# Optimization experiments

Hardware: AMD Instinct MI355X
Metric: run time of the kernel (lower is better)

Reference implementation:

```python
import jax, jax.numpy as jnp
import numpy as np

T, N, F, H, C, E, K = 8, 100000, 64, 64, 16, 1250000, 2


def setup_inputs() -> dict:
    key = jax.random.key(0)
    ks = jax.random.split(key, 18)
    s = 0.05
    inp = {
        'X_seq': jax.random.normal(ks[0], (T, N, F), jnp.float32),
        'edge_index': jax.random.randint(ks[1], (2, E), 0, N, dtype=jnp.int64),
    }
    # 6 ChebConvs: (x_z, h_z, x_r, h_r, x_h, h_h); weight (K, in, out), bias (out,)
    names_in = [('Wxz', F), ('Whz', H), ('Wxr', F), ('Whr', H), ('Wxh', F), ('Whh', H)]
    for i, (nm, cin) in enumerate(names_in):
        inp[nm] = jax.random.normal(ks[2 + 2 * i], (K, cin, H), jnp.float32) * s
        inp['b' + nm[1:]] = jnp.zeros((H,), jnp.float32)
    inp['Wlin'] = jax.random.normal(ks[14], (H, C), jnp.float32) * s
    inp['blin'] = jnp.zeros((C,), jnp.float32)
    return inp


def _cheb(x, W, b, mv):
    # ChebConv, sym normalization, lambda_max=2: L_tilde = -D^{-1/2} A D^{-1/2}
    out = x @ W[0]
    if W.shape[0] > 1:
        Tx_prev, Tx = x, mv(x)
        out = out + Tx @ W[1]
        for k in range(2, W.shape[0]):
            Tx_prev, Tx = Tx, 2.0 * mv(Tx) - Tx_prev
            out = out + Tx @ W[k]
    return out + b


def reference(X_seq, edge_index, Wxz, bxz, Whz, bhz, Wxr, bxr, Whr, bhr,
              Wxh, bxh, Whh, bhh, Wlin, blin):
    src, dst = edge_index[0], edge_index[1]
    n = X_seq.shape[1]
    deg = jax.ops.segment_sum(jnp.ones_like(src, jnp.float32), src, num_segments=n)
    dinv = jnp.where(deg > 0, jax.lax.rsqrt(jnp.maximum(deg, 1.0)), 0.0)
    w = -dinv[src] * dinv[dst]  # scaled Laplacian off-diagonal (diag is 0)

    def mv(x):  # L_tilde @ x via edge gather/scatter
        return jax.ops.segment_sum(w[:, None] * x[src], dst, num_segments=n)

    def step(h, x_t):
        z = jax.nn.sigmoid(_cheb(x_t, Wxz, bxz, mv) + _cheb(h, Whz, bhz, mv))
        r = jax.nn.sigmoid(_cheb(x_t, Wxr, bxr, mv) + _cheb(h, Whr, bhr, mv))
        h_tilde = jnp.tanh(_cheb(x_t, Wxh, bxh, mv) + _cheb(h * r, Whh, bhh, mv))
        h = z * h + (1.0 - z) * h_tilde
        return h, None

    h0 = jnp.zeros((n, Whz.shape[2]), X_seq.dtype)
    h, _ = jax.lax.scan(step, h0, X_seq)
    return h @ Wlin + blin
```

## Files before the change

kernel.cpp:

```cpp
#include <hip/hip_runtime.h>
#include <math.h>

#define T_STEPS 8
#define F_DIM 64

using half8 = __attribute__((ext_vector_type(8))) _Float16;
using half4 = __attribute__((ext_vector_type(4))) _Float16;
using f32x4 = __attribute__((ext_vector_type(4))) float;

__device__ __forceinline__ float sigmoidf_(float x) { return 1.f / (1.f + __expf(-x)); }


__global__ void k_deg_cnt(const int* ei, int E, int N, int* deg, int* cnt) {
  int e = blockIdx.x * blockDim.x + threadIdx.x;
  if (e >= E) return;
  int s = ei[e];
  int d = ei[E + e];
  if ((unsigned)s < (unsigned)N) atomicAdd(&deg[s], 1);
  if ((unsigned)d < (unsigned)N) atomicAdd(&cnt[d], 1);
}

__global__ void k_dinv(const int* deg, float* dinv, int n) {
  int i = blockIdx.x * blockDim.x + threadIdx.x;
  if (i >= n) return;
  int d = deg[i];
  dinv[i] = d > 0 ? 1.0f / sqrtf((float)d) : 0.f;
}

__global__ void k_scan1(const int* cnt, int* incl, int* bsum, int n) {
  __shared__ int s[1024];
  int t = threadIdx.x;
  int i = blockIdx.x * 1024 + t;
  int v = (i < n) ? cnt[i] : 0;
  s[t] = v;
  __syncthreads();
  for (int off = 1; off < 1024; off <<= 1) {
    int add = (t >= off) ? s[t - off] : 0;
    __syncthreads();
    s[t] += add;
    __syncthreads();
  }
  if (i < n) incl[i] = s[t];
  if (t == 1023) bsum[blockIdx.x] = s[1023];
}

__global__ void k_scan2(const int* bsum, int* boff, int nb) {
  if (threadIdx.x == 0 && blockIdx.x == 0) {
    int run = 0;
    for (int b = 0; b < nb; ++b) { int v = bsum[b]; boff[b] = run; run += v; }
  }
}

__global__ void k_scan3(const int* incl, const int* cnt, const int* boff,
                        int* rp, int n, int E) {
  int i = blockIdx.x * 1024 + threadIdx.x;
  if (i >= n) return;
  int b = i >> 10;
  rp[i] = incl[i] - cnt[i] + boff[b];
  if (i == n - 1) rp[n] = incl[i] + boff[b];
}

__global__ void k_fill(const int* ei, int E, int N, const float* dinv,
                       const int* rp, int* fill, int* col, float* wv) {
  int e = blockIdx.x * blockDim.x + threadIdx.x;
  if (e >= E) return;
  int s = ei[e];
  int d = ei[E + e];
  if ((unsigned)s >= (unsigned)N || (unsigned)d >= (unsigned)N) return;
  int pos = atomicAdd(&fill[d], 1);
  int j = rp[d] + pos;
  col[j] = s;
  wv[j] = -dinv[s] * dinv[d];
}

__global__ void k_pack(const float* Whz, const float* Whr, const float* Wxz, const float* Wxr,
                       const float* Whh, const float* Wxh,
                       const float* bhz, const float* bhr, const float* bxz, const float* bxr,
                       const float* bhh, const float* bxh,
                       _Float16* Wzr, _Float16* Wh2, float* bzr, float* bhb) {
  int i = blockIdx.x * 256 + threadIdx.x;
  if (i < 49152) {
    int q, chunk;
    const float *srcH, *srcX;
    _Float16* dst;
    if (i < 32768) {
      chunk = i >> 14;
      q = i & 16383;
      srcH = chunk == 0 ? Whz : Whr;
      srcX = chunk == 0 ? Wxz : Wxr;
      dst = Wzr + i;
    } else {
      q = i - 32768;
      srcH = Whh;
      srcX = Wxh;
      dst = Wh2 + q;
    }
    int e = q & 7, lq = (q >> 3) & 63, kk = (q >> 9) & 7, c = (q >> 12) & 3;
    int K = kk * 32 + ((lq >> 4) << 3) + e;
    int colg = c * 16 + (lq & 15);
    int m = K >> 6, row = K & 63, kidx = m & 1;
    const float* src = (m < 2) ? srcH : srcX;
    *dst = (_Float16)src[kidx * 4096 + row * 64 + colg];
  } else if (i < 49152 + 128) {
    int o = i - 49152;
    bzr[o] = (o < 64) ? (bhz[o] + bxz[o]) : (bhr[o - 64] + bxr[o - 64]);
  } else if (i < 49152 + 128 + 64) {
    int o = i - (49152 + 128);
    bhb[o] = bhh[o] + bxh[o];
  }
}

__global__ __launch_bounds__(256) void k_cvt_x(const float* __restrict__ X, _Float16* __restrict__ xh,
                                               int N, int total) {
  int i = blockIdx.x * 256 + threadIdx.x;
  if (i >= total) return;
  int per_t = N * 16;
  int t = i / per_t;
  int rem = i - t * per_t;
  int n = rem >> 4;
  int f4 = rem & 15;
  float4 v = *(const float4*)(X + (((size_t)t * N + n) << 6) + (f4 << 2));
  half4 o;
  o[0] = (_Float16)v.x; o[1] = (_Float16)v.y; o[2] = (_Float16)v.z; o[3] = (_Float16)v.w;
  *(half4*)(xh + ((size_t)n * (T_STEPS * 64)) + t * 64 + (f4 << 2)) = o;
}

__global__ __launch_bounds__(256) void k_spmv_x8(const int* __restrict__ rp,
                                                 const int* __restrict__ col,
                                                 const float* __restrict__ wv,
                                                 const _Float16* __restrict__ xh,
                                                 _Float16* __restrict__ y, int n) {
  int row = blockIdx.x * 4 + (threadIdx.x >> 6);
  if (row >= n) return;
  const int l = threadIdx.x & 63;
  const int off0 = l << 2;
  int s = rp[row], e = rp[row + 1];
  f32x4 a0 = {0.f, 0.f, 0.f, 0.f}, a1 = {0.f, 0.f, 0.f, 0.f};
  int j = s;
  for (; j + 2 <= e; j += 2) {
    int c0 = col[j], c1 = col[j + 1];
    float w0 = wv[j], w1 = wv[j + 1];
    const _Float16* p0 = xh + ((size_t)c0 << 9);
    const _Float16* p1 = xh + ((size_t)c1 << 9);
    half4 u0 = *(const half4*)(p0 + off0);
    half4 u1 = *(const half4*)(p0 + 256 + off0);
    half4 v0 = *(const half4*)(p1 + off0);
    half4 v1 = *(const half4*)(p1 + 256 + off0);
#pragma unroll
    for (int q = 0; q < 4; ++q) {
      a0[q] = fmaf(w0, (float)u0[q], a0[q]);
      a1[q] = fmaf(w0, (float)u1[q], a1[q]);
      a0[q] = fmaf(w1, (float)v0[q], a0[q]);
      a1[q] = fmaf(w1, (float)v1[q], a1[q]);
    }
  }
  if (j < e) {
    int c0 = col[j];
    float w0 = wv[j];
    const _Float16* p0 = xh + ((size_t)c0 << 9);
    half4 u0 = *(const half4*)(p0 + off0);
    half4 u1 = *(const half4*)(p0 + 256 + off0);
#pragma unroll
    for (int q = 0; q < 4; ++q) {
      a0[q] = fmaf(w0, (float)u0[q], a0[q]);
      a1[q] = fmaf(w0, (float)u1[q], a1[q]);
    }
  }
  _Float16* yp = y + ((size_t)row << 9);
  half4 o0, o1;
#pragma unroll
  for (int q = 0; q < 4; ++q) { o0[q] = (_Float16)a0[q]; o1[q] = (_Float16)a1[q]; }
  *(half4*)(yp + off0) = o0;
  *(half4*)(yp + 256 + off0) = o1;
}

__global__ __launch_bounds__(256) void k_spmv4(const int* __restrict__ rp,
                                               const int* __restrict__ col,
                                               const float* __restrict__ wv,
                                               const _Float16* __restrict__ x,
                                               _Float16* __restrict__ y, int n) {
  int row = blockIdx.x * 4 + (threadIdx.x >> 6);
  if (row >= n) return;
  const int l = threadIdx.x & 63;
  const int grp = l >> 4;
  const int foff = (l & 15) << 2;
  const int s = rp[row], e = rp[row + 1];
  f32x4 acc = {0.f, 0.f, 0.f, 0.f};
  for (int j0 = s + grp; j0 < e; j0 += 8) {
    int c0 = col[j0];
    float w0 = wv[j0];
    int j1 = j0 + 4;
    bool ok1 = j1 < e;
    int c1 = ok1 ? col[j1] : c0;
    float w1 = ok1 ? wv[j1] : 0.f;
    half4 u0 = *(const half4*)(x + ((size_t)c0 << 6) + foff);
    half4 u1 = *(const half4*)(x + ((size_t)c1 << 6) + foff);
#pragma unroll
    for (int q = 0; q < 4; ++q) {
      acc[q] = fmaf(w0, (float)u0[q], acc[q]);
      acc[q] = fmaf(w1, (float)u1[q], acc[q]);
    }
  }
#pragma unroll
  for (int q = 0; q < 4; ++q) {
    acc[q] += __shfl_xor(acc[q], 16);
    acc[q] += __shfl_xor(acc[q], 32);
  }
  if (grp == 0) {
    half4 o;
#pragma unroll
    for (int q = 0; q < 4; ++q) o[q] = (_Float16)acc[q];
    *(half4*)(y + ((size_t)row << 6) + foff) = o;
  }
}

__global__ __launch_bounds__(256) void k_spmv_f32(const int* __restrict__ rp,
                                                  const int* __restrict__ col,
                                                  const float* __restrict__ wv,
                                                  const float* __restrict__ x,
                                                  _Float16* __restrict__ y, int n) {
  int row = blockIdx.x * 4 + (threadIdx.x >> 6);
  if (row >= n) return;
  int lane = threadIdx.x & 63;
  int s = rp[row], e = rp[row + 1];
  float acc = 0.f, acc2 = 0.f;
  int j = s;
  for (; j + 2 <= e; j += 2) {
    acc = fmaf(wv[j], x[(size_t)col[j] * 64 + lane], acc);
    acc2 = fmaf(wv[j + 1], x[(size_t)col[j + 1] * 64 + lane], acc2);
  }
  if (j < e) acc = fmaf(wv[j], x[(size_t)col[j] * 64 + lane], acc);
  y[(size_t)row * 64 + lane] = (_Float16)(acc + acc2);
}

__global__ __launch_bounds__(256) void k_cvt1(const float* __restrict__ in,
                                              _Float16* __restrict__ o, int total4) {
  int i = blockIdx.x * 256 + threadIdx.x;
  if (i >= total4) return;
  float4 v = ((const float4*)in)[i];
  half4 h;
  h[0] = (_Float16)v.x; h[1] = (_Float16)v.y; h[2] = (_Float16)v.z; h[3] = (_Float16)v.w;
  ((half4*)o)[i] = h;
}

template <int EPI>
__global__ __launch_bounds__(256) void k_gmfma(
    const _Float16* __restrict__ A0, const _Float16* __restrict__ A1,
    const _Float16* __restrict__ A2, int s2, const _Float16* __restrict__ A3, int s3,
    const _Float16* __restrict__ Wpk, const float* __restrict__ bias,
    _Float16* __restrict__ zh, float* __restrict__ h, _Float16* __restrict__ hh,
    _Float16* __restrict__ hrh, int n) {
  const int t = threadIdx.x;
  const int l = t & 63;
  const int w = t >> 6;
  const int rh = w >> 1;
  const int ch = w & 1;
  const int rowBase = blockIdx.x * 64;
  const int chunk = (EPI == 0) ? blockIdx.y : 0;

  const _Float16* Wp = Wpk + (size_t)chunk * 16384;
  half8 bf[8][2];
#pragma unroll
  for (int kk = 0; kk < 8; ++kk)
#pragma unroll
    for (int cc = 0; cc < 2; ++cc)
      bf[kk][cc] = *(const half8*)(Wp + ((((ch * 2 + cc) * 8 + kk) * 64 + l) << 3));

  const int row0 = rowBase + rh * 32 + (l & 15);
  const int row1 = row0 + 16;
  const bool r0ok = row0 < n, r1ok = row1 < n;

  f32x4 acc[2][2] = {};
#pragma unroll
  for (int kk = 0; kk < 8; ++kk) {
    const int m = kk >> 1;
    const int coloff = (kk & 1) * 32 + ((l >> 4) << 3);
    const _Float16* base = (m == 0) ? A0 : (m == 1) ? A1 : (m == 2) ? A2 : A3;
    const int st = (m <= 1) ? 64 : (m == 2 ? s2 : s3);
    half8 a0{}, a1{};
    if (r0ok) a0 = *(const half8*)(base + (size_t)row0 * st + coloff);
    if (r1ok) a1 = *(const half8*)(base + (size_t)row1 * st + coloff);
#pragma unroll
    for (int cc = 0; cc < 2; ++cc) {
      acc[0][cc] = __builtin_amdgcn_mfma_f32_16x16x32_f16(a0, bf[kk][cc], acc[0][cc], 0, 0, 0);
      acc[1][cc] = __builtin_amdgcn_mfma_f32_16x16x32_f16(a1, bf[kk][cc], acc[1][cc], 0, 0, 0);
    }
  }

#pragma unroll
  for (int rt = 0; rt < 2; ++rt)
#pragma unroll
    for (int cc = 0; cc < 2; ++cc) {
      const int colg = ch * 32 + cc * 16 + (l & 15);
      const float b = bias[chunk * 64 + colg];
#pragma unroll
      for (int reg = 0; reg < 4; ++reg) {
        const int row = rowBase + rh * 32 + rt * 16 + ((l >> 4) << 2) + reg;
        if (row >= n) continue;
        const float s = acc[rt][cc][reg] + b;
        const size_t idx = ((size_t)row << 6) + colg;
        if (EPI == 0) {
          const float g = sigmoidf_(s);
          if (chunk == 0) zh[idx] = (_Float16)g;
          else hrh[idx] = (_Float16)(h[idx] * g);
        } else {
          const float ht = tanhf(s);
          const float zz = (float)zh[idx];
          const float hn = zz * h[idx] + (1.f - zz) * ht;
          h[idx] = hn;
          hh[idx] = (_Float16)hn;
        }
      }
    }
}

__global__ __launch_bounds__(256) void k_lin(const float* __restrict__ h,
                                             const float* __restrict__ Wlin,
                                             const float* __restrict__ blin,
                                             float* __restrict__ out, int n) {
  __shared__ float Wl[64 * 16];
  __shared__ float bl[16];
  int t = threadIdx.x;
#pragma unroll
  for (int it = 0; it < 4; ++it) Wl[it * 256 + t] = Wlin[it * 256 + t];
  if (t < 16) bl[t] = blin[t];
  __syncthreads();
  int r = blockIdx.x * 16 + (t >> 4);
  int c = t & 15;
  if (r >= n) return;
  const float* hp = h + (size_t)r * 64;
  float acc = bl[c];
#pragma unroll
  for (int k = 0; k < 64; ++k) acc = fmaf(hp[k], Wl[k * 16 + c], acc);
  out[(size_t)r * 16 + c] = acc;
}

extern "C" void kernel_launch(void* const* d_in, const int* in_sizes, int n_in,
                              void* d_out, int out_size, void* d_ws, size_t ws_size,
                              hipStream_t stream) {
  const float* Xseq = (const float*)d_in[0];
  const int* ei = (const int*)d_in[1];
  const float* Wxz = (const float*)d_in[2];
  const float* bxz = (const float*)d_in[3];
  const float* Whz = (const float*)d_in[4];
  const float* bhz = (const float*)d_in[5];
  const float* Wxr = (const float*)d_in[6];
  const float* bxr = (const float*)d_in[7];
  const float* Whr = (const float*)d_in[8];
  const float* bhr = (const float*)d_in[9];
  const float* Wxh = (const float*)d_in[10];
  const float* bxh = (const float*)d_in[11];
  const float* Whh = (const float*)d_in[12];
  const float* bhh = (const float*)d_in[13];
  const float* Wlin = (const float*)d_in[14];
  const float* blin = (const float*)d_in[15];
  float* out = (float*)d_out;

  const int N = in_sizes[0] / (T_STEPS * F_DIM);
  const int E = in_sizes[1] / 2;

  char* p = (char*)d_ws;
  size_t used = 0;
  auto alloc = [&](size_t bytes) {
    char* r = p;
    size_t a = (bytes + 255) & ~(size_t)255;
    p += a;
    used += a;
    return r;
  };
  int* deg = (int*)alloc((size_t)N * 4);
  int* cnt = (int*)alloc((size_t)N * 4);
  int* incl = (int*)alloc((size_t)N * 4);
  int* fill = (int*)alloc((size_t)N * 4);
  int* bsum = (int*)alloc(512 * 4);
  int* boff = (int*)alloc(512 * 4);
  float* dinv = (float*)alloc((size_t)N * 4);
  int* rp = (int*)alloc((size_t)(N + 1) * 4);
  int* col = (int*)alloc((size_t)E * 4);
  float* wv = (float*)alloc((size_t)E * 4);
  _Float16* Wzr = (_Float16*)alloc(32768 * 2);
  _Float16* Wh2 = (_Float16*)alloc(16384 * 2);
  float* bzr = (float*)alloc(128 * 4);
  float* bhb = (float*)alloc(64 * 4);
  float* h = (float*)alloc((size_t)N * 64 * 4);
  _Float16* hh = (_Float16*)alloc((size_t)N * 64 * 2);
  _Float16* mv2h = (_Float16*)alloc((size_t)N * 64 * 2);
  _Float16* hrh = (_Float16*)alloc((size_t)N * 64 * 2);
  _Float16* zh = (_Float16*)alloc((size_t)N * 64 * 2);

  size_t need_big = 2 * ((size_t)N * T_STEPS * 64 * 2 + 255);
  bool big = (used + need_big + 4096) <= ws_size;
  _Float16 *xh_i = nullptr, *mvx_i = nullptr, *xth = nullptr, *mvxth = nullptr;
  if (big) {
    xh_i = (_Float16*)alloc((size_t)N * T_STEPS * 64 * 2);
    mvx_i = (_Float16*)alloc((size_t)N * T_STEPS * 64 * 2);
  } else {
    xth = (_Float16*)alloc((size_t)N * 64 * 2);
    mvxth = (_Float16*)alloc((size_t)N * 64 * 2);
  }

  hipMemsetAsync(deg, 0, (size_t)N * 4, stream);
  hipMemsetAsync(cnt, 0, (size_t)N * 4, stream);
  hipMemsetAsync(fill, 0, (size_t)N * 4, stream);
  hipMemsetAsync(h, 0, (size_t)N * 64 * 4, stream);
  hipMemsetAsync(hh, 0, (size_t)N * 64 * 2, stream);

  k_deg_cnt<<<(E + 255) / 256, 256, 0, stream>>>(ei, E, N, deg, cnt);
  k_dinv<<<(N + 255) / 256, 256, 0, stream>>>(deg, dinv, N);
  int nb = (N + 1023) / 1024;
  k_scan1<<<nb, 1024, 0, stream>>>(cnt, incl, bsum, N);
  k_scan2<<<1, 1, 0, stream>>>(bsum, boff, nb);
  k_scan3<<<nb, 1024, 0, stream>>>(incl, cnt, boff, rp, N, E);
  k_fill<<<(E + 255) / 256, 256, 0, stream>>>(ei, E, N, dinv, rp, fill, col, wv);
  k_pack<<<(49152 + 192 + 255) / 256, 256, 0, stream>>>(Whz, Whr, Wxz, Wxr, Whh, Wxh,
                                                        bhz, bhr, bxz, bxr, bhh, bxh,
                                                        Wzr, Wh2, bzr, bhb);

  if (big) {
    int total = T_STEPS * N * 16;
    k_cvt_x<<<(total + 255) / 256, 256, 0, stream>>>(Xseq, xh_i, N, total);
    k_spmv_x8<<<(N + 3) / 4, 256, 0, stream>>>(rp, col, wv, xh_i, mvx_i, N);
  }

  const int gb = (N + 63) / 64;
  for (int tt = 0; tt < T_STEPS; ++tt) {
    const float* xt = Xseq + (size_t)tt * N * F_DIM;
    const _Float16* A2;
    const _Float16* A3;
    int s2, s3;
    if (big) {
      A2 = xh_i + tt * 64; s2 = T_STEPS * 64;
      A3 = mvx_i + tt * 64; s3 = T_STEPS * 64;
    } else {
      k_cvt1<<<(N * 16 + 255) / 256, 256, 0, stream>>>(xt, xth, N * 16);
      k_spmv_f32<<<(N + 3) / 4, 256, 0, stream>>>(rp, col, wv, xt, mvxth, N);
      A2 = xth; s2 = 64;
      A3 = mvxth; s3 = 64;
    }
    k_spmv4<<<(N + 3) / 4, 256, 0, stream>>>(rp, col, wv, hh, mv2h, N);
    dim3 gzr(gb, 2);
    k_gmfma<0><<<gzr, 256, 0, stream>>>(hh, mv2h, A2, s2, A3, s3, Wzr, bzr,
                                        zh, h, hh, hrh, N);
    k_spmv4<<<(N + 3) / 4, 256, 0, stream>>>(rp, col, wv, hrh, mv2h, N);
    dim3 gh(gb, 1);
    k_gmfma<1><<<gh, 256, 0, stream>>>(hrh, mv2h, A2, s2, A3, s3, Wh2, bhb,
                                       zh, h, hh, hrh, N);
  }
  k_lin<<<(N + 15) / 16, 256, 0, stream>>>(h, Wlin, blin, out, N);
}
```

Baseline: 2.079 ms.

## Pack CSR col/weight into int2, parallelize block-offset scan, merge z/r GEMM blocks

Interleaves column index and edge weight into a single int2 array so every SpMV reads one 8-byte load per edge instead of two separate streams. Replaces the single-thread block-offset scan with a 1024-thread shared-memory scan. Stores the precomputed L·x in a time-major layout so the per-step GEMM reads a contiguous 64-wide stride. Splits the templated GEMM into a 512-thread z/r kernel that computes both gates in one block and a separate h kernel. The z/r merge raises registers per block, which may lower occupancy.

After: 2.114 ms. No clear change (+1.7%).

```diff
diff --git a/kernel.cpp b/kernel.cpp
--- a/kernel.cpp
+++ b/kernel.cpp
@@ -44,6 +44,21 @@
   if (t == 1023) bsum[blockIdx.x] = s[1023];
 }
 
+__global__ void k_scan2p(const int* bsum, int* boff, int nb) {
+  __shared__ int sh[1024];
+  int t = threadIdx.x;
+  int v = (t < nb) ? bsum[t] : 0;
+  sh[t] = v;
+  __syncthreads();
+  for (int off = 1; off < 1024; off <<= 1) {
+    int add = (t >= off) ? sh[t - off] : 0;
+    __syncthreads();
+    sh[t] += add;
+    __syncthreads();
+  }
+  if (t < nb) boff[t] = sh[t] - v;
+}
+
 __global__ void k_scan2(const int* bsum, int* boff, int nb) {
   if (threadIdx.x == 0 && blockIdx.x == 0) {
     int run = 0;
@@ -61,7 +76,7 @@
 }
 
 __global__ void k_fill(const int* ei, int E, int N, const float* dinv,
-                       const int* rp, int* fill, int* col, float* wv) {
+                       const int* rp, int* fill, int2* cw) {
   int e = blockIdx.x * blockDim.x + threadIdx.x;
   if (e >= E) return;
   int s = ei[e];
@@ -69,8 +84,10 @@
   if ((unsigned)s >= (unsigned)N || (unsigned)d >= (unsigned)N) return;
   int pos = atomicAdd(&fill[d], 1);
   int j = rp[d] + pos;
-  col[j] = s;
-  wv[j] = -dinv[s] * dinv[d];
+  int2 v;
+  v.x = s;
+  v.y = __float_as_int(-dinv[s] * dinv[d]);
+  cw[j] = v;
 }
 
 __global__ void k_pack(const float* Whz, const float* Whr, const float* Wxz, const float* Wxr,
@@ -126,8 +143,7 @@
 }
 
 __global__ __launch_bounds__(256) void k_spmv_x8(const int* __restrict__ rp,
-                                                 const int* __restrict__ col,
-                                                 const float* __restrict__ wv,
+                                                 const int2* __restrict__ cw,
                                                  const _Float16* __restrict__ xh,
                                                  _Float16* __restrict__ y, int n) {
   int row = blockIdx.x * 4 + (threadIdx.x >> 6);
@@ -138,45 +154,45 @@
   f32x4 a0 = {0.f, 0.f, 0.f, 0.f}, a1 = {0.f, 0.f, 0.f, 0.f};
   int j = s;
   for (; j + 2 <= e; j += 2) {
-    int c0 = col[j], c1 = col[j + 1];
-    float w0 = wv[j], w1 = wv[j + 1];
-    const _Float16* p0 = xh + ((size_t)c0 << 9);
-    const _Float16* p1 = xh + ((size_t)c1 << 9);
+    int2 p = cw[j], q = cw[j + 1];
+    float w0 = __int_as_float(p.y), w1 = __int_as_float(q.y);
+    const _Float16* p0 = xh + ((size_t)p.x << 9);
+    const _Float16* p1 = xh + ((size_t)q.x << 9);
     half4 u0 = *(const half4*)(p0 + off0);
     half4 u1 = *(const half4*)(p0 + 256 + off0);
     half4 v0 = *(const half4*)(p1 + off0);
     half4 v1 = *(const half4*)(p1 + 256 + off0);
 #pragma unroll
-    for (int q = 0; q < 4; ++q) {
-      a0[q] = fmaf(w0, (float)u0[q], a0[q]);
-      a1[q] = fmaf(w0, (float)u1[q], a1[q]);
-      a0[q] = fmaf(w1, (float)v0[q], a0[q]);
-      a1[q] = fmaf(w1, (float)v1[q], a1[q]);
+    for (int qq = 0; qq < 4; ++qq) {
+      a0[qq] = fmaf(w0, (float)u0[qq], a0[qq]);
+      a1[qq] = fmaf(w0, (float)u1[qq], a1[qq]);
+      a0[qq] = fmaf(w1, (float)v0[qq], a0[qq]);
+      a1[qq] = fmaf(w1, (float)v1[qq], a1[qq]);
     }
   }
   if (j < e) {
-    int c0 = col[j];
-    float w0 = wv[j];
-    const _Float16* p0 = xh + ((size_t)c0 << 9);
+    int2 p = cw[j];
+    float w0 = __int_as_float(p.y);
+    const _Float16* p0 = xh + ((size_t)p.x << 9);
     half4 u0 = *(const half4*)(p0 + off0);
     half4 u1 = *(const half4*)(p0 + 256 + off0);
 #pragma unroll
-    for (int q = 0; q < 4; ++q) {
-      a0[q] = fmaf(w0, (float)u0[q], a0[q]);
-      a1[q] = fmaf(w0, (float)u1[q], a1[q]);
-    }
-  }
-  _Float16* yp = y + ((size_t)row << 9);
+    for (int qq = 0; qq < 4; ++qq) {
+      a0[qq] = fmaf(w0, (float)u0[qq], a0[qq]);
+      a1[qq] = fmaf(w0, (float)u1[qq], a1[qq]);
+    }
+  }
+  const int t0 = l >> 4;
+  const int foff = (l & 15) << 2;
   half4 o0, o1;
 #pragma unroll
-  for (int q = 0; q < 4; ++q) { o0[q] = (_Float16)a0[q]; o1[q] = (_Float16)a1[q]; }
-  *(half4*)(yp + off0) = o0;
-  *(half4*)(yp + 256 + off0) = o1;
+  for (int qq = 0; qq < 4; ++qq) { o0[qq] = (_Float16)a0[qq]; o1[qq] = (_Float16)a1[qq]; }
+  *(half4*)(y + ((size_t)t0 * n << 6) + ((size_t)row << 6) + foff) = o0;
+  *(half4*)(y + ((size_t)(t0 + 4) * n << 6) + ((size_t)row << 6) + foff) = o1;
 }
 
 __global__ __launch_bounds__(256) void k_spmv4(const int* __restrict__ rp,
-                                               const int* __restrict__ col,
-                                               const float* __restrict__ wv,
+                                               const int2* __restrict__ cw,
                                                const _Float16* __restrict__ x,
                                                _Float16* __restrict__ y, int n) {
   int row = blockIdx.x * 4 + (threadIdx.x >> 6);
@@ -187,36 +203,35 @@
   const int s = rp[row], e = rp[row + 1];
   f32x4 acc = {0.f, 0.f, 0.f, 0.f};
   for (int j0 = s + grp; j0 < e; j0 += 8) {
-    int c0 = col[j0];
-    float w0 = wv[j0];
+    int2 p = cw[j0];
+    float w0 = __int_as_float(p.y);
     int j1 = j0 + 4;
     bool ok1 = j1 < e;
-    int c1 = ok1 ? col[j1] : c0;
-    float w1 = ok1 ? wv[j1] : 0.f;
-    half4 u0 = *(const half4*)(x + ((size_t)c0 << 6) + foff);
-    half4 u1 = *(const half4*)(x + ((size_t)c1 << 6) + foff);
-#pragma unroll
-    for (int q = 0; q < 4; ++q) {
-      acc[q] = fmaf(w0, (float)u0[q], acc[q]);
-      acc[q] = fmaf(w1, (float)u1[q], acc[q]);
-    }
-  }
-#pragma unroll
-  for (int q = 0; q < 4; ++q) {
-    acc[q] += __shfl_xor(acc[q], 16);
-    acc[q] += __shfl_xor(acc[q], 32);
+    int2 q = ok1 ? cw[j1] : p;
+    float w1 = ok1 ? __int_as_float(q.y) : 0.f;
+    half4 u0 = *(const half4*)(x + ((size_t)p.x << 6) + foff);
+    half4 u1 = *(const half4*)(x + ((size_t)q.x << 6) + foff);
+#pragma unroll
+    for (int qq = 0; qq < 4; ++qq) {
+      acc[qq] = fmaf(w0, (float)u0[qq], acc[qq]);
+      acc[qq] = fmaf(w1, (float)u1[qq], acc[qq]);
+    }
+  }
+#pragma unroll
+  for (int qq = 0; qq < 4; ++qq) {
+    acc[qq] += __shfl_xor(acc[qq], 16);
+    acc[qq] += __shfl_xor(acc[qq], 32);
   }
   if (grp == 0) {
     half4 o;
 #pragma unroll
-    for (int q = 0; q < 4; ++q) o[q] = (_Float16)acc[q];
+    for (int qq = 0; qq < 4; ++qq) o[qq] = (_Float16)acc[qq];
     *(half4*)(y + ((size_t)row << 6) + foff) = o;
   }
 }
 
 __global__ __launch_bounds__(256) void k_spmv_f32(const int* __restrict__ rp,
-                                                  const int* __restrict__ col,
-                                                  const float* __restrict__ wv,
+                                                  const int2* __restrict__ cw,
                                                   const float* __restrict__ x,
                                                   _Float16* __restrict__ y, int n) {
   int row = blockIdx.x * 4 + (threadIdx.x >> 6);
@@ -226,10 +241,14 @@
   float acc = 0.f, acc2 = 0.f;
   int j = s;
   for (; j + 2 <= e; j += 2) {
-    acc = fmaf(wv[j], x[(size_t)col[j] * 64 + lane], acc);
-    acc2 = fmaf(wv[j + 1], x[(size_t)col[j + 1] * 64 + lane], acc2);
-  }
-  if (j < e) acc = fmaf(wv[j], x[(size_t)col[j] * 64 + lane], acc);
+    int2 p = cw[j], q = cw[j + 1];
+    acc = fmaf(__int_as_float(p.y), x[(size_t)p.x * 64 + lane], acc);
+    acc2 = fmaf(__int_as_float(q.y), x[(size_t)q.x * 64 + lane], acc2);
+  }
+  if (j < e) {
+    int2 p = cw[j];
+    acc = fmaf(__int_as_float(p.y), x[(size_t)p.x * 64 + lane], acc);
+  }
   y[(size_t)row * 64 + lane] = (_Float16)(acc + acc2);
 }
 
@@ -243,20 +262,18 @@
   ((half4*)o)[i] = h;
 }
 
-template <int EPI>
-__global__ __launch_bounds__(256) void k_gmfma(
+__global__ __launch_bounds__(512) void k_gzr(
     const _Float16* __restrict__ A0, const _Float16* __restrict__ A1,
     const _Float16* __restrict__ A2, int s2, const _Float16* __restrict__ A3, int s3,
     const _Float16* __restrict__ Wpk, const float* __restrict__ bias,
-    _Float16* __restrict__ zh, float* __restrict__ h, _Float16* __restrict__ hh,
-    _Float16* __restrict__ hrh, int n) {
+    _Float16* __restrict__ zh, float* __restrict__ h, _Float16* __restrict__ hrh, int n) {
   const int t = threadIdx.x;
   const int l = t & 63;
   const int w = t >> 6;
-  const int rh = w >> 1;
+  const int chunk = w >> 2;
+  const int rh = (w >> 1) & 1;
   const int ch = w & 1;
   const int rowBase = blockIdx.x * 64;
-  const int chunk = (EPI == 0) ? blockIdx.y : 0;
 
   const _Float16* Wp = Wpk + (size_t)chunk * 16384;
   half8 bf[8][2];
@@ -297,19 +314,72 @@
       for (int reg = 0; reg < 4; ++reg) {
         const int row = rowBase + rh * 32 + rt * 16 + ((l >> 4) << 2) + reg;
         if (row >= n) continue;
-        const float s = acc[rt][cc][reg] + b;
+        const float sv = acc[rt][cc][reg] + b;
         const size_t idx = ((size_t)row << 6) + colg;
-        if (EPI == 0) {
-          const float g = sigmoidf_(s);
-          if (chunk == 0) zh[idx] = (_Float16)g;
-          else hrh[idx] = (_Float16)(h[idx] * g);
-        } else {
-          const float ht = tanhf(s);
-          const float zz = (float)zh[idx];
-          const float hn = zz * h[idx] + (1.f - zz) * ht;
-          h[idx] = hn;
-          hh[idx] = (_Float16)hn;
-        }
+        const float g = sigmoidf_(sv);
+        if (chunk == 0) zh[idx] = (_Float16)g;
+        else hrh[idx] = (_Float16)(h[idx] * g);
+      }
+    }
+}
+
+__global__ __launch_bounds__(256) void k_gh(
+    const _Float16* __restrict__ A0, const _Float16* __restrict__ A1,
+    const _Float16* __restrict__ A2, int s2, const _Float16* __restrict__ A3, int s3,
+    const _Float16* __restrict__ Wpk, const float* __restrict__ bias,
+    const _Float16* __restrict__ zh, float* __restrict__ h, _Float16* __restrict__ hh, int n) {
+  const int t = threadIdx.x;
+  const int l = t & 63;
+  const int w = t >> 6;
+  const int rh = w >> 1;
+  const int ch = w & 1;
+  const int rowBase = blockIdx.x * 64;
+
+  half8 bf[8][2];
+#pragma unroll
+  for (int kk = 0; kk < 8; ++kk)
+#pragma unroll
+    for (int cc = 0; cc < 2; ++cc)
+      bf[kk][cc] = *(const half8*)(Wpk + ((((ch * 2 + cc) * 8 + kk) * 64 + l) << 3));
+
+  const int row0 = rowBase + rh * 32 + (l & 15);
+  const int row1 = row0 + 16;
+  const bool r0ok = row0 < n, r1ok = row1 < n;
+
+  f32x4 acc[2][2] = {};
+#pragma unroll
+  for (int kk = 0; kk < 8; ++kk) {
+    const int m = kk >> 1;
+    const int coloff = (kk & 1) * 32 + ((l >> 4) << 3);
+    const _Float16* base = (m == 0) ? A0 : (m == 1) ? A1 : (m == 2) ? A2 : A3;
+    const int st = (m <= 1) ? 64 : (m == 2 ? s2 : s3);
+    half8 a0{}, a1{};
+    if (r0ok) a0 = *(const half8*)(base + (size_t)row0 * st + coloff);
+    if (r1ok) a1 = *(const half8*)(base + (size_t)row1 * st + coloff);
+#pragma unroll
+    for (int cc = 0; cc < 2; ++cc) {
+      acc[0][cc] = __builtin_amdgcn_mfma_f32_16x16x32_f16(a0, bf[kk][cc], acc[0][cc], 0, 0, 0);
+      acc[1][cc] = __builtin_amdgcn_mfma_f32_16x16x32_f16(a1, bf[kk][cc], acc[1][cc], 0, 0, 0);
+    }
+  }
+
+#pragma unroll
+  for (int rt = 0; rt < 2; ++rt)
+#pragma unroll
+    for (int cc = 0; cc < 2; ++cc) {
+      const int colg = ch * 32 + cc * 16 + (l & 15);
+      const float b = bias[colg];
+#pragma unroll
+      for (int reg = 0; reg < 4; ++reg) {
+        const int row = rowBase + rh * 32 + rt * 16 + ((l >> 4) << 2) + reg;
+        if (row >= n) continue;
+        const float sv = acc[rt][cc][reg] + b;
+        const size_t idx = ((size_t)row << 6) + colg;
+        const float ht = tanhf(sv);
+        const float zz = (float)zh[idx];
+        const float hn = zz * h[idx] + (1.f - zz) * ht;
+        h[idx] = hn;
+        hh[idx] = (_Float16)hn;
       }
     }
 }
@@ -372,12 +442,11 @@
   int* cnt = (int*)alloc((size_t)N * 4);
   int* incl = (int*)alloc((size_t)N * 4);
   int* fill = (int*)alloc((size_t)N * 4);
-  int* bsum = (int*)alloc(512 * 4);
-  int* boff = (int*)alloc(512 * 4);
+  int* bsum = (int*)alloc(1024 * 4);
+  int* boff = (int*)alloc(1024 * 4);
   float* dinv = (float*)alloc((size_t)N * 4);
   int* rp = (int*)alloc((size_t)(N + 1) * 4);
-  int* col = (int*)alloc((size_t)E * 4);
-  float* wv = (float*)alloc((size_t)E * 4);
+  int2* cw = (int2*)alloc((size_t)E * 8);
   _Float16* Wzr = (_Float16*)alloc(32768 * 2);
   _Float16* Wh2 = (_Float16*)alloc(16384 * 2);
   float* bzr = (float*)alloc(128 * 4);
@@ -390,10 +459,10 @@
 
   size_t need_big = 2 * ((size_t)N * T_STEPS * 64 * 2 + 255);
   bool big = (used + need_big + 4096) <= ws_size;
-  _Float16 *xh_i = nullptr, *mvx_i = nullptr, *xth = nullptr, *mvxth = nullptr;
+  _Float16 *xh_i = nullptr, *mvx_t = nullptr, *xth = nullptr, *mvxth = nullptr;
   if (big) {
     xh_i = (_Float16*)alloc((size_t)N * T_STEPS * 64 * 2);
-    mvx_i = (_Float16*)alloc((size_t)N * T_STEPS * 64 * 2);
+    mvx_t = (_Float16*)alloc((size_t)T_STEPS * N * 64 * 2);
   } else {
     xth = (_Float16*)alloc((size_t)N * 64 * 2);
     mvxth = (_Float16*)alloc((size_t)N * 64 * 2);
@@ -409,9 +478,12 @@
   k_dinv<<<(N + 255) / 256, 256, 0, stream>>>(deg, dinv, N);
   int nb = (N + 1023) / 1024;
   k_scan1<<<nb, 1024, 0, stream>>>(cnt, incl, bsum, N);
-  k_scan2<<<1, 1, 0, stream>>>(bsum, boff, nb);
+  if (nb <= 1024)
+    k_scan2p<<<1, 1024, 0, stream>>>(bsum, boff, nb);
+  else
+    k_scan2<<<1, 1, 0, stream>>>(bsum, boff, nb);
   k_scan3<<<nb, 1024, 0, stream>>>(incl, cnt, boff, rp, N, E);
-  k_fill<<<(E + 255) / 256, 256, 0, stream>>>(ei, E, N, dinv, rp, fill, col, wv);
+  k_fill<<<(E + 255) / 256, 256, 0, stream>>>(ei, E, N, dinv, rp, fill, cw);
   k_pack<<<(49152 + 192 + 255) / 256, 256, 0, stream>>>(Whz, Whr, Wxz, Wxr, Whh, Wxh,
                                                         bhz, bhr, bxz, bxr, bhh, bxh,
                                                         Wzr, Wh2, bzr, bhb);
@@ -419,7 +491,7 @@
   if (big) {
     int total = T_STEPS * N * 16;
     k_cvt_x<<<(total + 255) / 256, 256, 0, stream>>>(Xseq, xh_i, N, total);
-    k_spmv_x8<<<(N + 3) / 4, 256, 0, stream>>>(rp, col, wv, xh_i, mvx_i, N);
+    k_spmv_x8<<<(N + 3) / 4, 256, 0, stream>>>(rp, cw, xh_i, mvx_t, N);
   }
 
   const int gb = (N + 63) / 64;
@@ -430,21 +502,17 @@
     int s2, s3;
     if (big) {
       A2 = xh_i + tt * 64; s2 = T_STEPS * 64;
-      A3 = mvx_i + tt * 64; s3 = T_STEPS * 64;
+      A3 = mvx_t + (size_t)tt * N * 64; s3 = 64;
     } else {
       k_cvt1<<<(N * 16 + 255) / 256, 256, 0, stream>>>(xt, xth, N * 16);
-      k_spmv_f32<<<(N + 3) / 4, 256, 0, stream>>>(rp, col, wv, xt, mvxth, N);
+      k_spmv_f32<<<(N + 3) / 4, 256, 0, stream>>>(rp, cw, xt, mvxth, N);
       A2 = xth; s2 = 64;
       A3 = mvxth; s3 = 64;
     }
-    k_spmv4<<<(N + 3) / 4, 256, 0, stream>>>(rp, col, wv, hh, mv2h, N);
-    dim3 gzr(gb, 2);
-    k_gmfma<0><<<gzr, 256, 0, stream>>>(hh, mv2h, A2, s2, A3, s3, Wzr, bzr,
-                                        zh, h, hh, hrh, N);
-    k_spmv4<<<(N + 3) / 4, 256, 0, stream>>>(rp, col, wv, hrh, mv2h, N);
-    dim3 gh(gb, 1);
-    k_gmfma<1><<<gh, 256, 0, stream>>>(hrh, mv2h, A2, s2, A3, s3, Wh2, bhb,
-                                       zh, h, hh, hrh, N);
+    k_spmv4<<<(N + 3) / 4, 256, 0, stream>>>(rp, cw, hh, mv2h, N);
+    k_gzr<<<gb, 512, 0, stream>>>(hh, mv2h, A2, s2, A3, s3, Wzr, bzr, zh, h, hrh, N);
+    k_spmv4<<<(N + 3) / 4, 256, 0, stream>>>(rp, cw, hrh, mv2h, N);
+    k_gh<<<gb, 256, 0, stream>>>(hrh, mv2h, A2, s2, A3, s3, Wh2, bhb, zh, h, hh, N);
   }
   k_lin<<<(N + 15) / 16, 256, 0, stream>>>(h, Wlin, blin, out, N);
 }
```
